# Kernel optimization log

Hardware: AMD Instinct MI355X
Metric: run time of the kernel (lower is better)

The kernel has to match this reference:

```python
import jax, jax.numpy as jnp
import numpy as np
from functools import partial

B, S, V, H, NH, NKV, M, L = 2, 2048, 51200, 1536, 24, 4, 8960, 8
DH = H // NH  # 64
EPS = 1e-6


def setup_inputs() -> dict:
    key = jax.random.key(0)
    ks = jax.random.split(key, 16)
    sc = 0.02
    w = lambda k, shape: jax.random.normal(k, shape, jnp.float32) * sc
    inp = {
        "input_ids": jax.random.randint(ks[0], (B, S), 0, V),
        "attention_mask": jnp.ones((B, S), jnp.float32),
        "embed": w(ks[1], (V, H)),
        "Wq": w(ks[2], (L, H, H)),          "bq": jnp.zeros((L, H), jnp.float32),
        "Wk": w(ks[3], (L, H, NKV * DH)),   "bk": jnp.zeros((L, NKV * DH), jnp.float32),
        "Wv": w(ks[4], (L, H, NKV * DH)),   "bv": jnp.zeros((L, NKV * DH), jnp.float32),
        "Wo": w(ks[5], (L, H, H)),
        "ln1": jnp.ones((L, H), jnp.float32),
        "ln2": jnp.ones((L, H), jnp.float32),
        "Wg": w(ks[6], (L, H, M)),
        "Wu": w(ks[7], (L, H, M)),
        "Wd": w(ks[8], (L, M, H)),
        "norm_w": jnp.ones((H,), jnp.float32),
        "W1": w(ks[9], (H, H)), "b1": jnp.zeros((H,), jnp.float32),
        "W2": w(ks[10], (H, 1)), "b2": jnp.zeros((1,), jnp.float32),
    }
    inv_freq = 1.0 / (10000.0 ** (jnp.arange(0, DH, 2, dtype=jnp.float32) / DH))
    freqs = jnp.outer(jnp.arange(S, dtype=jnp.float32), inv_freq)  # [S, DH/2]
    emb = jnp.concatenate([freqs, freqs], axis=-1)                 # [S, DH]
    inp["cos"] = jnp.cos(emb)
    inp["sin"] = jnp.sin(emb)
    return inp


def _rms(x, w):
    var = jnp.mean(x.astype(jnp.float32) ** 2, axis=-1, keepdims=True)
    return w * (x * jax.lax.rsqrt(var + EPS)).astype(x.dtype)


def _rotate_half(x):
    x1, x2 = jnp.split(x, 2, axis=-1)
    return jnp.concatenate([-x2, x1], axis=-1)


def _forward(input_ids, attention_mask, embed, Wq, bq, Wk, bk, Wv, bv, Wo,
             ln1, ln2, Wg, Wu, Wd, norm_w, W1, b1, W2, b2, cos, sin):
    scale = 1.0 / np.sqrt(DH)
    b, s = input_ids.shape
    c = cos[None, :s, None, :]  # [1,S,1,DH]
    sn = sin[None, :s, None, :]
    rope = lambda t: t * c + _rotate_half(t) * sn
    mask0 = attention_mask[:, None, None, :] == 0  # [B,1,1,S]

    def block(x, p):
        wq, bq_, wk, bk_, wv, bv_, wo, ln1w, ln2w, wg, wu, wd = p
        h = _rms(x, ln1w)
        q = (h @ wq + bq_).reshape(b, s, NH, DH)
        k = (h @ wk + bk_).reshape(b, s, NKV, DH)
        v = (h @ wv + bv_).reshape(b, s, NKV, DH)
        q, k = rope(q), rope(k)
        k = jnp.repeat(k, NH // NKV, axis=2)  # GQA expand to NH heads
        v = jnp.repeat(v, NH // NKV, axis=2)
        scores = jnp.einsum('bqhd,bkhd->bhqk', q, k) * scale
        scores = jnp.where(mask0, -1e10, scores)
        probs = jax.nn.softmax(scores, axis=-1)  # dropout: eval mode (identity)
        attn = jnp.einsum('bhqk,bkhd->bqhd', probs, v).reshape(b, s, H)
        x = x + attn @ wo
        h = _rms(x, ln2w)
        x = x + (jax.nn.sigmoid(h @ wg) * (h @ wu)) @ wd
        return x, None

    x = embed[input_ids]  # [B,S,H]
    x, _ = jax.lax.scan(block, x, (Wq, bq, Wk, bk, Wv, bv, Wo, ln1, ln2, Wg, Wu, Wd))
    x = _rms(x, norm_w)
    h = jax.nn.gelu(x @ W1 + b1, approximate=False)  # torch nn.GELU default = exact
    return h @ W2 + b2  # [B,S,1]


def reference(input_ids, attention_mask, embed, Wq, bq, Wk, bk, Wv, bv, Wo,
              ln1, ln2, Wg, Wu, Wd, norm_w, W1, b1, W2, b2, cos, sin):
    return _forward(input_ids, attention_mask, embed, Wq, bq, Wk, bk, Wv, bv, Wo,
                    ln1, ln2, Wg, Wu, Wd, norm_w, W1, b1, W2, b2, cos, sin)
```

## Files before the change

kernel.cpp:

```cpp
#include <hip/hip_runtime.h>

typedef float f32x4 __attribute__((ext_vector_type(4)));
typedef short s16x8 __attribute__((ext_vector_type(8)));
typedef unsigned short u16;
typedef unsigned short u16x4 __attribute__((ext_vector_type(4)));
typedef unsigned short u16x8 __attribute__((ext_vector_type(8)));
typedef unsigned int u32x2 __attribute__((ext_vector_type(2)));

__device__ __forceinline__ float bf2f(u16 u){ union{unsigned int i; float f;} v; v.i=((unsigned int)u)<<16; return v.f; }
__device__ __forceinline__ u16 f2bf(float f){ union{float f; unsigned int i;} v; v.f=f; return (u16)((v.i + 0x7FFFu + ((v.i>>16)&1u))>>16); }
__device__ __forceinline__ float aexp2(float x){ float r; asm("v_exp_f32 %0, %1" : "=v"(r) : "v"(x)); return r; }
__device__ __forceinline__ unsigned int cvtpk(float lo, float hi){ unsigned int r; asm("v_cvt_pk_bf16_f32 %0, %1, %2" : "=v"(r) : "v"(lo), "v"(hi)); return r; }

#define LOG2E 1.44269504089f

__device__ __forceinline__ void gld16(const void* gp, void* lp){
  __builtin_amdgcn_global_load_lds((__attribute__((address_space(1))) void*)(void*)gp,
                                   (__attribute__((address_space(3))) void*)lp, 16, 0, 0);
}

__global__ __launch_bounds__(256) void k_embed(const int* __restrict__ ids, const float* __restrict__ emb, float* __restrict__ x){
  int r = blockIdx.x;
  int id = ids[r];
  const f32x4* src = (const f32x4*)(emb + (size_t)id*1536);
  f32x4* dst = (f32x4*)(x + (size_t)r*1536);
  for (int i = threadIdx.x; i < 384; i += 256) dst[i] = src[i];
}

__global__ __launch_bounds__(256) void k_rms(const float* __restrict__ x, const float* __restrict__ w, u16* __restrict__ h){
  int r = blockIdx.x, tid = threadIdx.x;
  const f32x4* xr = (const f32x4*)(x + (size_t)r*1536);
  f32x4 v0 = xr[tid];
  float ss = v0.x*v0.x + v0.y*v0.y + v0.z*v0.z + v0.w*v0.w;
  f32x4 v1 = {0,0,0,0};
  if (tid < 128){ v1 = xr[256+tid]; ss += v1.x*v1.x + v1.y*v1.y + v1.z*v1.z + v1.w*v1.w; }
  #pragma unroll
  for (int off=32; off; off>>=1) ss += __shfl_xor(ss, off, 64);
  __shared__ float red[4];
  if ((tid&63)==0) red[tid>>6] = ss;
  __syncthreads();
  float tot = red[0]+red[1]+red[2]+red[3];
  float invr = rsqrtf(tot*(1.f/1536.f) + 1e-6f);
  const f32x4* w4 = (const f32x4*)w;
  u16x4* h4 = (u16x4*)(h + (size_t)r*1536);
  {
    f32x4 wv = w4[tid];
    u16x4 o; o.x=f2bf(v0.x*invr*wv.x); o.y=f2bf(v0.y*invr*wv.y); o.z=f2bf(v0.z*invr*wv.z); o.w=f2bf(v0.w*invr*wv.w);
    h4[tid] = o;
  }
  if (tid < 128){
    f32x4 wv = w4[256+tid];
    u16x4 o; o.x=f2bf(v1.x*invr*wv.x); o.y=f2bf(v1.y*invr*wv.y); o.z=f2bf(v1.z*invr*wv.z); o.w=f2bf(v1.w*invr*wv.w);
    h4[256+tid] = o;
  }
}

__global__ __launch_bounds__(256) void k_rms_add(float* __restrict__ x, const float* __restrict__ P, const float* __restrict__ w, u16* __restrict__ h){
  int r = blockIdx.x, tid = threadIdx.x;
  f32x4* xr = (f32x4*)(x + (size_t)r*1536);
  const f32x4* pr = (const f32x4*)(P + (size_t)r*1536);
  f32x4 v0 = xr[tid], p0 = pr[tid];
  v0.x+=p0.x; v0.y+=p0.y; v0.z+=p0.z; v0.w+=p0.w;
  xr[tid] = v0;
  float ss = v0.x*v0.x + v0.y*v0.y + v0.z*v0.z + v0.w*v0.w;
  f32x4 v1 = {0,0,0,0};
  if (tid < 128){
    v1 = xr[256+tid]; f32x4 p1 = pr[256+tid];
    v1.x+=p1.x; v1.y+=p1.y; v1.z+=p1.z; v1.w+=p1.w;
    xr[256+tid] = v1;
    ss += v1.x*v1.x + v1.y*v1.y + v1.z*v1.z + v1.w*v1.w;
  }
  #pragma unroll
  for (int off=32; off; off>>=1) ss += __shfl_xor(ss, off, 64);
  __shared__ float red[4];
  if ((tid&63)==0) red[tid>>6] = ss;
  __syncthreads();
  float tot = red[0]+red[1]+red[2]+red[3];
  float invr = rsqrtf(tot*(1.f/1536.f) + 1e-6f);
  const f32x4* w4 = (const f32x4*)w;
  u16x4* h4 = (u16x4*)(h + (size_t)r*1536);
  {
    f32x4 wv = w4[tid];
    u16x4 o; o.x=f2bf(v0.x*invr*wv.x); o.y=f2bf(v0.y*invr*wv.y); o.z=f2bf(v0.z*invr*wv.z); o.w=f2bf(v0.w*invr*wv.w);
    h4[tid] = o;
  }
  if (tid < 128){
    f32x4 wv = w4[256+tid];
    u16x4 o; o.x=f2bf(v1.x*invr*wv.x); o.y=f2bf(v1.y*invr*wv.y); o.z=f2bf(v1.z*invr*wv.z); o.w=f2bf(v1.w*invr*wv.w);
    h4[256+tid] = o;
  }
}

__device__ __forceinline__ void cvt_tile(const float* src, int K, int N, u16* dst, int k0, int n0, int roff, int mode){
  __shared__ float T[64*72];
  int tid = threadIdx.x;
  #pragma unroll
  for (int j=0;j<4;++j){
    int i = tid + j*256;
    int row = i>>4, nf = i&15;
    f32x4 vv = *(const f32x4*)(src + (size_t)(k0+row)*N + n0 + nf*4);
    *(f32x4*)&T[row*72 + nf*4] = vv;
  }
  __syncthreads();
  #pragma unroll
  for (int j=0;j<2;++j){
    int i = tid + j*256;
    int n = i>>3, kc = i&7;
    u16x8 o;
    #pragma unroll
    for (int m=0;m<8;++m) o[m] = f2bf(T[(kc*8+m)*72 + n]);
    int gn = n0 + n;
    int dr = (mode==0) ? (roff + gn) : (((gn>>4)<<5) + ((mode==2)?16:0) + (gn&15));
    *(u16x8*)(dst + (size_t)dr*K + k0 + kc*8) = o;
  }
}

__global__ __launch_bounds__(256) void k_cvt_layer(
  const float* __restrict__ Wq, const float* __restrict__ Wk, const float* __restrict__ Wv,
  const float* __restrict__ Wo, const float* __restrict__ Wg, const float* __restrict__ Wu,
  const float* __restrict__ Wd, u16* qkvt, u16* wot, u16* gut, u16* wdt)
{
  const float* src; int K, N; u16* dst; int roff=0, mode=0;
  switch (blockIdx.y){
    case 0: src=Wq; K=1536; N=1536; dst=qkvt; break;
    case 1: src=Wk; K=1536; N=256;  dst=qkvt; roff=1536; break;
    case 2: src=Wv; K=1536; N=256;  dst=qkvt; roff=1792; break;
    case 3: src=Wo; K=1536; N=1536; dst=wot;  break;
    case 4: src=Wg; K=1536; N=8960; dst=gut;  mode=1; break;
    case 5: src=Wu; K=1536; N=8960; dst=gut;  mode=2; break;
    default: src=Wd; K=8960; N=1536; dst=wdt; break;
  }
  int ntn = N>>6;
  int nt = (K>>6)*ntn;
  int t = blockIdx.x;
  if (t >= nt) return;
  cvt_tile(src, K, N, dst, (t/ntn)<<6, (t%ntn)<<6, roff, mode);
}

__global__ __launch_bounds__(256) void k_cvt_one(const float* __restrict__ src, u16* __restrict__ dst){
  int t = blockIdx.x;
  cvt_tile(src, 1536, 1536, dst, (t/24)<<6, (t%24)<<6, 0, 0);
}

#define MODE_QKV 0
#define MODE_WO 1
#define MODE_GATEUP 2
#define MODE_DOWN 3
#define MODE_W1 4

template<int MODE>
__global__ __launch_bounds__(256) void k_gemm(
  const u16* __restrict__ A, const u16* __restrict__ Bt, int K,
  int jobsPerXcd, int nc, int ksplit, int klen,
  const float* __restrict__ bq_, const float* __restrict__ bk_, const float* __restrict__ bv_,
  float* __restrict__ xio, float* __restrict__ Pf,
  const float* __restrict__ cosT, const float* __restrict__ sinT,
  u16* __restrict__ o0, u16* __restrict__ o1, u16* __restrict__ o2)
{
  int bid = blockIdx.x;
  int xcd = bid & 7, j = bid >> 3;
  int job = xcd*jobsPerXcd + (j >> 5);
  if (job >= nc*ksplit) return;
  int rowb = j & 31;
  int col = job / ksplit;
  int ks  = job - col*ksplit;
  int kbase = ks*klen;
  int nt = klen >> 5;

  __shared__ __align__(16) u16 As[4][4096], Bs[4][4096];
  int tid = threadIdx.x;
  int lane = tid & 63, w = tid >> 6;
  int wr = w >> 1, wc = w & 1;
  int row0 = rowb * 128, col0 = col * 128;
  int l15 = lane & 15, l4 = lane >> 4;
  f32x4 acc[4][4] = {};
  const u16* aBase = A + (size_t)row0*K;
  const u16* bBase = Bt + (size_t)col0*K;
  int rr0 = tid & 127, kb0 = tid >> 7;
  int kb1 = kb0 + 2;

  auto stage = [&](int bf, int kt){
    gld16(aBase + (size_t)rr0*K + kt + kb0*8, &As[bf][tid*8]);
    gld16(bBase + (size_t)rr0*K + kt + kb0*8, &Bs[bf][tid*8]);
    gld16(aBase + (size_t)rr0*K + kt + kb1*8, &As[bf][(256+tid)*8]);
    gld16(bBase + (size_t)rr0*K + kt + kb1*8, &Bs[bf][(256+tid)*8]);
  };
  stage(0, kbase); stage(1, kbase+32); stage(2, kbase+64);

  for (int t = 0; t < nt; ++t){
    if (t < nt-2)       asm volatile("s_waitcnt vmcnt(8)" ::: "memory");
    else if (t == nt-2) asm volatile("s_waitcnt vmcnt(4)" ::: "memory");
    else                asm volatile("s_waitcnt vmcnt(0)" ::: "memory");
    __builtin_amdgcn_s_barrier();
    __builtin_amdgcn_sched_barrier(0);
    if (t+3 < nt) stage((t+3)&3, kbase + (t+3)*32);
    const u16* Ab = As[t&3];
    const u16* Bb = Bs[t&3];
    s16x8 af[4], bf_[4];
    #pragma unroll
    for (int i=0;i<4;++i) af[i]  = *(const s16x8*)&Ab[((l4<<7) + wr*64 + i*16 + l15)*8];
    #pragma unroll
    for (int jj=0;jj<4;++jj) bf_[jj] = *(const s16x8*)&Bb[((l4<<7) + wc*64 + jj*16 + l15)*8];
    __builtin_amdgcn_s_setprio(1);
    #pragma unroll
    for (int i=0;i<4;++i)
      #pragma unroll
      for (int jj=0;jj<4;++jj)
        acc[i][jj] = __builtin_amdgcn_mfma_f32_16x16x32_bf16(af[i], bf_[jj], acc[i][jj], 0, 0, 0);
    __builtin_amdgcn_s_setprio(0);
  }

  #pragma unroll
  for (int i=0;i<4;++i)
    #pragma unroll
    for (int jj=0;jj<4;++jj)
      #pragma unroll
      for (int r=0;r<4;++r){
        int row = row0 + wr*64 + i*16 + l4*4 + r;
        int c   = col0 + wc*64 + jj*16 + l15;
        float v = acc[i][jj][r];
        if constexpr (MODE == MODE_QKV){
          int b = row >> 11, s = row & 2047;
          if (c < 1536){
            int d = c & 63, hd = c >> 6;
            float vv = v + bq_[c];
            float pv = acc[i][jj^2][r] + bq_[c^32];
            float cv = cosT[s*64+d], sv = sinT[s*64+d];
            float sgn = (d<32) ? -1.f : 1.f;
            float o = (vv*cv + sgn*pv*sv)*(0.125f*LOG2E);
            o0[(size_t)(b*24+hd)*131072 + (size_t)(s>>6)*4096
               + (s&63)*64 + (((d>>3)^(s&7))<<3) + (d&7)] = f2bf(o);
          } else if (c < 1792){
            int c2 = c - 1536, d = c2 & 63, kv = c2 >> 6;
            float vv = v + bk_[c2];
            float pv = acc[i][jj^2][r] + bk_[c2^32];
            float cv = cosT[s*64+d], sv = sinT[s*64+d];
            float sgn = (d<32) ? -1.f : 1.f;
            float o = vv*cv + sgn*pv*sv;
            o1[(size_t)(b*4+kv)*131072 + (size_t)(s>>6)*4096
               + (s&63)*64 + (((d>>3)^(s&7))<<3) + (d&7)] = f2bf(o);
          } else {
            int c2 = c - 1792, d = c2 & 63, kv = c2 >> 6;
            float vv = v + bv_[c2];
            o2[(size_t)(b*4+kv)*131072 + (size_t)(s>>6)*4096
               + d*64 + ((((s>>3)&7)^(d&7))<<3) + (s&7)] = f2bf(vv);
          }
        } else if constexpr (MODE == MODE_WO){
          xio[(size_t)row*1536 + c] += v;
        } else if constexpr (MODE == MODE_W1){
          v += bq_[c];
          float ge = 0.5f * v * (1.f + erff(v * 0.70710678118f));
          o0[(size_t)row*1536 + c] = f2bf(ge);
        }
      }
}

template<int MODE>
__global__ __launch_bounds__(512,2) void k_gemm256(
  const u16* __restrict__ A, const u16* __restrict__ Bt, int K,
  int nrt, int ksplit, int klen,
  float* __restrict__ xio, float* __restrict__ Pf, u16* __restrict__ o0)
{
  int bid = blockIdx.x;
  int wgid = (bid & 7)*(gridDim.x >> 3) + (bid >> 3);
  int nj = nrt*ksplit;
  int ct = wgid / nj; int r2 = wgid - ct*nj;
  int rt = r2 / ksplit; int ks = r2 - rt*ksplit;

  __shared__ __align__(16) u16 lds[2][2][16384];
  int tid = threadIdx.x;
  int lane = tid & 63, wid = tid >> 6;
  int wm = wid >> 2, wn = wid & 3;
  int l15 = lane & 15, l4 = lane >> 4;
  int row0 = rt*256, col0 = ct*256;
  int kbase = ks*klen*64;

  const u16* aB = A  + (size_t)row0*K + kbase;
  const u16* bB = Bt + (size_t)col0*K + kbase;
  int rsub = tid >> 3;
  int gsw  = (lane & 7) ^ ((lane >> 3) & 7);

  f32x4 acc[8][4] = {};

  auto stage = [&](int bf, int ktElem){
    #pragma unroll
    for (int a_=0; a_<4; ++a_){
      gld16(aB + (size_t)(a_*64 + rsub)*K + ktElem + gsw*8, &lds[bf][0][(a_*512+tid)*8]);
      gld16(bB + (size_t)(a_*64 + rsub)*K + ktElem + gsw*8, &lds[bf][1][(a_*512+tid)*8]);
    }
  };

  stage(0, 0);
  for (int t = 0; t < klen; ++t){
    asm volatile("s_waitcnt vmcnt(0)" ::: "memory");
    __builtin_amdgcn_s_barrier();
    __builtin_amdgcn_sched_barrier(0);
    if (t+1 < klen) stage((t+1)&1, (t+1)*64);
    const u16* Ab = lds[t&1][0];
    const u16* Bb = lds[t&1][1];
    #pragma unroll
    for (int ksu=0; ksu<2; ++ksu){
      s16x8 af[8], bf_[4];
      #pragma unroll
      for (int i=0;i<8;++i){
        int r = wm*128 + i*16 + l15;
        af[i] = *(const s16x8*)&Ab[r*64 + (((ksu*4 + l4) ^ (l15&7))*8)];
      }
      #pragma unroll
      for (int j=0;j<4;++j){
        int c = wn*64 + j*16 + l15;
        bf_[j] = *(const s16x8*)&Bb[c*64 + (((ksu*4 + l4) ^ (l15&7))*8)];
      }
      __builtin_amdgcn_s_setprio(1);
      #pragma unroll
      for (int i=0;i<8;++i)
        #pragma unroll
        for (int j=0;j<4;++j)
          acc[i][j] = __builtin_amdgcn_mfma_f32_16x16x32_bf16(af[i], bf_[j], acc[i][j], 0, 0, 0);
      __builtin_amdgcn_s_setprio(0);
    }
  }

  if constexpr (MODE == MODE_GATEUP){
    #pragma unroll
    for (int i=0;i<8;++i)
      #pragma unroll
      for (int j2=0;j2<4;j2+=2)
        #pragma unroll
        for (int r=0;r<4;++r){
          int row = row0 + wm*128 + i*16 + l4*4 + r;
          int cp  = col0 + wn*64 + j2*16 + l15;
          float gv = acc[i][j2][r], uv = acc[i][j2+1][r];
          float sg = 1.f/(1.f + __expf(-gv));
          int n = ((cp>>5)<<4) + (cp&15);
          o0[(size_t)row*8960 + n] = f2bf(sg*uv);
        }
  } else {
    #pragma unroll
    for (int i=0;i<8;++i)
      #pragma unroll
      for (int j=0;j<4;++j)
        #pragma unroll
        for (int r=0;r<4;++r){
          int row = row0 + wm*128 + i*16 + l4*4 + r;
          int c   = col0 + wn*64 + j*16 + l15;
          float v = acc[i][j][r];
          if (ks == 0) Pf[(size_t)row*1536 + c] = v;
          else         xio[(size_t)row*1536 + c] += v;
        }
  }
}

__global__ __launch_bounds__(256) void k_attn(
  const u16* __restrict__ q, const u16* __restrict__ k, const u16* __restrict__ v,
  const float* __restrict__ mask, u16* __restrict__ attn)
{
  __shared__ __align__(16) u16 Qs[4096];
  __shared__ __align__(16) u16 Kd[2][4096];
  __shared__ __align__(16) u16 Vd[2][4096];
  __shared__ u16 Msh[2048];
  int tid = threadIdx.x;
  int lane = tid & 63, w = tid >> 6;
  int qb = blockIdx.x;
  int bh = blockIdx.y;
  int b = bh / 24, hh = bh % 24, kv = hh / 6;
  int l15 = lane & 15, l4 = lane >> 4;
  int sw = l15 & 7;

  const u16* qhead = q + ((size_t)(b*24 + hh))*131072 + qb*4096;
  const u16* khead = k + ((size_t)(b*4  + kv))*131072;
  const u16* vhead = v + ((size_t)(b*4  + kv))*131072;

  {
    const f32x4* m4 = (const f32x4*)(mask + b*2048);
    const u16 mvis = f2bf(-4.f*LOG2E);
    const u16 mmask = f2bf(-1.4e9f);
    for (int i = tid; i < 512; i += 256){
      f32x4 mv = m4[i];
      u16x4 o;
      o.x = (mv.x==0.f) ? mmask : mvis;
      o.y = (mv.y==0.f) ? mmask : mvis;
      o.z = (mv.z==0.f) ? mmask : mvis;
      o.w = (mv.w==0.f) ? mmask : mvis;
      *(u16x4*)&Msh[i*4] = o;
    }
  }
  gld16(qhead + tid*8,       &Qs[tid*8]);
  gld16(qhead + (256+tid)*8, &Qs[(256+tid)*8]);

  auto stage = [&](int bf, int kt){
    gld16(khead + kt*4096 + tid*8,       &Kd[bf][tid*8]);
    gld16(khead + kt*4096 + (256+tid)*8, &Kd[bf][(256+tid)*8]);
    gld16(vhead + kt*4096 + tid*8,       &Vd[bf][tid*8]);
    gld16(vhead + kt*4096 + (256+tid)*8, &Vd[bf][(256+tid)*8]);
  };
  stage(0, 0);

  s16x8 aq0, aq1;
  f32x4 oacc[4] = {};
  float lsum = 0.f;
  u16* Pw = &Qs[w*1024];

  for (int t = 0; t < 32; ++t){
    asm volatile("s_waitcnt vmcnt(0)" ::: "memory");
    __builtin_amdgcn_s_barrier();
    __builtin_amdgcn_sched_barrier(0);
    if (t == 0){
      int qrow = w*16 + l15;
      aq0 = *(const s16x8*)&Qs[qrow*64 + (( l4    ^ sw)<<3)];
      aq1 = *(const s16x8*)&Qs[qrow*64 + (((4+l4) ^ sw)<<3)];
    }
    if (t+1 < 32) stage((t+1)&1, t+1);
    const u16* Kb = Kd[t&1];
    const u16* Vb = Vd[t&1];
    f32x4 sk[4] = {};
    __builtin_amdgcn_s_setprio(1);
    #pragma unroll
    for (int kn=0; kn<4; ++kn){
      int krow = kn*16 + l15;
      s16x8 a0 = *(const s16x8*)&Kb[krow*64 + (( l4    ^ sw)<<3)];
      s16x8 a1 = *(const s16x8*)&Kb[krow*64 + (((4+l4) ^ sw)<<3)];
      sk[kn] = __builtin_amdgcn_mfma_f32_16x16x32_bf16(a0, aq0, sk[kn], 0,0,0);
      sk[kn] = __builtin_amdgcn_mfma_f32_16x16x32_bf16(a1, aq1, sk[kn], 0,0,0);
    }
    __builtin_amdgcn_s_setprio(0);
    #pragma unroll
    for (int kn=0; kn<4; ++kn){
      u16x4 mv = *(const u16x4*)&Msh[t*64 + kn*16 + l4*4];
      float p0 = aexp2(sk[kn][0] + bf2f(mv.x));
      float p1 = aexp2(sk[kn][1] + bf2f(mv.y));
      float p2 = aexp2(sk[kn][2] + bf2f(mv.z));
      float p3 = aexp2(sk[kn][3] + bf2f(mv.w));
      lsum += (p0 + p1) + (p2 + p3);
      u32x2 pk; pk.x = cvtpk(p0, p1); pk.y = cvtpk(p2, p3);
      int g = kn*2 + (l4>>1);
      *(u32x2*)&Pw[l15*64 + ((g ^ sw)<<3) + (l4&1)*4] = pk;
    }
    __builtin_amdgcn_s_setprio(1);
    #pragma unroll
    for (int ksu=0; ksu<2; ++ksu){
      s16x8 ap = *(const s16x8*)&Pw[l15*64 + (((ksu*4+l4) ^ sw)<<3)];
      #pragma unroll
      for (int dg=0; dg<4; ++dg){
        s16x8 bv = *(const s16x8*)&Vb[(dg*16+l15)*64 + (((ksu*4+l4) ^ sw)<<3)];
        oacc[dg] = __builtin_amdgcn_mfma_f32_16x16x32_bf16(ap, bv, oacc[dg], 0,0,0);
      }
    }
    __builtin_amdgcn_s_setprio(0);
  }
  lsum += __shfl_xor(lsum, 16, 64);
  lsum += __shfl_xor(lsum, 32, 64);
  float invq[4];
  #pragma unroll
  for (int r=0;r<4;++r) invq[r] = 1.f / __shfl(lsum, l4*4 + r, 64);
  #pragma unroll
  for (int dg=0;dg<4;++dg)
    #pragma unroll
    for (int r=0;r<4;++r){
      int token = b*2048 + qb*64 + w*16 + l4*4 + r;
      int col = hh*64 + dg*16 + l15;
      attn[(size_t)token*1536 + col] = f2bf(oacc[dg][r] * invq[r]);
    }
}

__global__ __launch_bounds__(256) void k_gemv(const u16* __restrict__ h2, const float* __restrict__ W2, const float* __restrict__ b2, float* __restrict__ out){
  int tid = threadIdx.x, lane = tid & 63, w = tid >> 6;
  int r = blockIdx.x*4 + w;
  const u16* hr = h2 + (size_t)r*1536;
  float s = 0.f;
  #pragma unroll
  for (int i=0;i<24;++i){ int c = lane + i*64; s += bf2f(hr[c]) * W2[c]; }
  #pragma unroll
  for (int off=32; off; off>>=1) s += __shfl_xor(s, off, 64);
  if (lane == 0) out[r] = s + b2[0];
}

extern "C" void kernel_launch(void* const* d_in, const int* in_sizes, int n_in,
                              void* d_out, int out_size, void* d_ws, size_t ws_size,
                              hipStream_t stream)
{
  const int*   ids   = (const int*)d_in[0];
  const float* mask  = (const float*)d_in[1];
  const float* embed = (const float*)d_in[2];
  const float* Wq    = (const float*)d_in[3];
  const float* bq    = (const float*)d_in[4];
  const float* Wk    = (const float*)d_in[5];
  const float* bk    = (const float*)d_in[6];
  const float* Wv    = (const float*)d_in[7];
  const float* bv    = (const float*)d_in[8];
  const float* Wo    = (const float*)d_in[9];
  const float* ln1   = (const float*)d_in[10];
  const float* ln2   = (const float*)d_in[11];
  const float* Wg    = (const float*)d_in[12];
  const float* Wu    = (const float*)d_in[13];
  const float* Wd    = (const float*)d_in[14];
  const float* nw    = (const float*)d_in[15];
  const float* W1    = (const float*)d_in[16];
  const float* b1    = (const float*)d_in[17];
  const float* W2    = (const float*)d_in[18];
  const float* b2    = (const float*)d_in[19];
  const float* cosT  = (const float*)d_in[20];
  const float* sinT  = (const float*)d_in[21];

  char* ws = (char*)d_ws;
  float* x   = (float*)(ws + 0);
  u16* h     = (u16*)(ws + 25165824);
  u16* qb_   = (u16*)(ws + 37748736);
  u16* kb_   = (u16*)(ws + 50331648);
  u16* vb_   = (u16*)(ws + 52428800);
  u16* attn  = (u16*)(ws + 54525952);
  u16* g     = (u16*)(ws + 67108864);
  u16* qkvt  = (u16*)(ws + 140509184);
  u16* wot   = (u16*)(ws + 146800640);
  u16* gut   = (u16*)(ws + 151519232);
  u16* wdt   = (u16*)(ws + 206569472);
  float* Pf  = (float*)(ws + 37748736);
  (void)in_sizes; (void)n_in; (void)out_size; (void)ws_size;

  k_embed<<<4096, 256, 0, stream>>>(ids, embed, x);
  for (int l = 0; l < 8; ++l){
    k_cvt_layer<<<dim3(3360,7), 256, 0, stream>>>(
      Wq + (size_t)l*1536*1536, Wk + (size_t)l*1536*256, Wv + (size_t)l*1536*256,
      Wo + (size_t)l*1536*1536, Wg + (size_t)l*1536*8960, Wu + (size_t)l*1536*8960,
      Wd + (size_t)l*8960*1536, qkvt, wot, gut, wdt);
    if (l == 0) k_rms<<<4096, 256, 0, stream>>>(x, ln1, h);
    else        k_rms_add<<<4096, 256, 0, stream>>>(x, Pf, ln1 + l*1536, h);
    k_gemm<MODE_QKV><<<512, 256, 0, stream>>>(h, qkvt, 1536, 2, 16, 1, 1536,
        bq + l*1536, bk + l*256, bv + l*256, nullptr, nullptr, cosT, sinT, qb_, kb_, vb_);
    k_attn<<<dim3(32,48), 256, 0, stream>>>(qb_, kb_, vb_, mask, attn);
    k_gemm<MODE_WO><<<512, 256, 0, stream>>>(attn, wot, 1536, 2, 12, 1, 1536,
        nullptr, nullptr, nullptr, x, nullptr, nullptr, nullptr, nullptr, nullptr, nullptr);
    k_rms<<<4096, 256, 0, stream>>>(x, ln2 + l*1536, h);
    k_gemm256<MODE_GATEUP><<<1120, 512, 0, stream>>>(h, gut, 1536, 16, 1, 24,
        nullptr, nullptr, g);
    k_gemm256<MODE_DOWN><<<192, 512, 0, stream>>>(g, wdt, 8960, 16, 2, 70,
        x, Pf, nullptr);
  }
  k_cvt_one<<<576, 256, 0, stream>>>(W1, wot);
  k_rms_add<<<4096, 256, 0, stream>>>(x, Pf, nw, h);
  k_gemm<MODE_W1><<<512, 256, 0, stream>>>(h, wot, 1536, 2, 12, 1, 1536,
      b1, nullptr, nullptr, nullptr, nullptr, nullptr, nullptr, attn, nullptr, nullptr);
  k_gemv<<<1024, 256, 0, stream>>>(attn, W2, b2, (float*)d_out);
}
```

Baseline: 5.425 ms.

## Split GEMM tile loads into chunks interleaved with MFMA phases using partial waitcnts

The 256x256 bf16 GEMM main loop no longer waits for all global-to-LDS loads before computing. The next k-tile's B and A loads are issued in quarter chunks between four MFMA sub-phases. Partial vmcnt waits plus a mid-iteration barrier let compute on the first A rows start while the rest are still arriving. The B fragments for both k-subtiles are kept in registers and the A fragments are loaded two row-blocks at a time. This aims to hide load latency and cut peak register use, at the cost of an extra barrier per iteration and fragile hand-counted waitcnt ordering.

```diff
diff --git a/kernel.cpp b/kernel.cpp
--- a/kernel.cpp
+++ b/kernel.cpp
@@ -272,6 +272,7 @@
   int lane = tid & 63, wid = tid >> 6;
   int wm = wid >> 2, wn = wid & 3;
   int l15 = lane & 15, l4 = lane >> 4;
+  int lsw = l15 & 7;
   int row0 = rt*256, col0 = ct*256;
   int kbase = ks*klen*64;
 
@@ -282,41 +283,109 @@
 
   f32x4 acc[8][4] = {};
 
-  auto stage = [&](int bf, int ktElem){
-    #pragma unroll
-    for (int a_=0; a_<4; ++a_){
-      gld16(aB + (size_t)(a_*64 + rsub)*K + ktElem + gsw*8, &lds[bf][0][(a_*512+tid)*8]);
-      gld16(bB + (size_t)(a_*64 + rsub)*K + ktElem + gsw*8, &lds[bf][1][(a_*512+tid)*8]);
-    }
+  auto sgA = [&](int bf, int kt, int c){
+    gld16(aB + (size_t)(c*64 + rsub)*K + kt*64 + gsw*8, &lds[bf][0][(c*512+tid)*8]);
   };
-
-  stage(0, 0);
+  auto sgB = [&](int bf, int kt, int c){
+    gld16(bB + (size_t)(c*64 + rsub)*K + kt*64 + gsw*8, &lds[bf][1][(c*512+tid)*8]);
+  };
+
+  sgB(0,0,0); sgB(0,0,1); sgB(0,0,2); sgB(0,0,3);
+  sgA(0,0,0); sgA(0,0,2); sgA(0,0,1); sgA(0,0,3);
+
   for (int t = 0; t < klen; ++t){
-    asm volatile("s_waitcnt vmcnt(0)" ::: "memory");
+    int b = t & 1, nb = b ^ 1;
+    bool hasNext = (t+1 < klen);
+    const u16* Ab = lds[b][0];
+    const u16* Bb = lds[b][1];
+
+    asm volatile("s_waitcnt vmcnt(2)" ::: "memory");
     __builtin_amdgcn_s_barrier();
     __builtin_amdgcn_sched_barrier(0);
-    if (t+1 < klen) stage((t+1)&1, (t+1)*64);
-    const u16* Ab = lds[t&1][0];
-    const u16* Bb = lds[t&1][1];
-    #pragma unroll
-    for (int ksu=0; ksu<2; ++ksu){
-      s16x8 af[8], bf_[4];
-      #pragma unroll
-      for (int i=0;i<8;++i){
-        int r = wm*128 + i*16 + l15;
-        af[i] = *(const s16x8*)&Ab[r*64 + (((ksu*4 + l4) ^ (l15&7))*8)];
-      }
-      #pragma unroll
-      for (int j=0;j<4;++j){
-        int c = wn*64 + j*16 + l15;
-        bf_[j] = *(const s16x8*)&Bb[c*64 + (((ksu*4 + l4) ^ (l15&7))*8)];
-      }
+    if (hasNext){ sgB(nb, t+1, 0); sgB(nb, t+1, 1); }
+
+    s16x8 bf_[4][2];
+    #pragma unroll
+    for (int j=0;j<4;++j)
+      #pragma unroll
+      for (int ksu=0;ksu<2;++ksu)
+        bf_[j][ksu] = *(const s16x8*)&Bb[(wn*64 + j*16 + l15)*64 + (((ksu*4+l4)^lsw)<<3)];
+
+    {
+      s16x8 af[2][2];
+      #pragma unroll
+      for (int ii=0;ii<2;++ii)
+        #pragma unroll
+        for (int ksu=0;ksu<2;++ksu)
+          af[ii][ksu] = *(const s16x8*)&Ab[(wm*128 + ii*16 + l15)*64 + (((ksu*4+l4)^lsw)<<3)];
       __builtin_amdgcn_s_setprio(1);
       #pragma unroll
-      for (int i=0;i<8;++i)
+      for (int ii=0;ii<2;++ii)
         #pragma unroll
         for (int j=0;j<4;++j)
-          acc[i][j] = __builtin_amdgcn_mfma_f32_16x16x32_bf16(af[i], bf_[j], acc[i][j], 0, 0, 0);
+          #pragma unroll
+          for (int ksu=0;ksu<2;++ksu)
+            acc[ii][j] = __builtin_amdgcn_mfma_f32_16x16x32_bf16(af[ii][ksu], bf_[j][ksu], acc[ii][j], 0,0,0);
+      __builtin_amdgcn_s_setprio(0);
+    }
+    if (hasNext){ sgB(nb, t+1, 2); sgB(nb, t+1, 3); }
+    {
+      s16x8 af[2][2];
+      #pragma unroll
+      for (int ii=0;ii<2;++ii)
+        #pragma unroll
+        for (int ksu=0;ksu<2;++ksu)
+          af[ii][ksu] = *(const s16x8*)&Ab[(wm*128 + 32 + ii*16 + l15)*64 + (((ksu*4+l4)^lsw)<<3)];
+      __builtin_amdgcn_s_setprio(1);
+      #pragma unroll
+      for (int ii=0;ii<2;++ii)
+        #pragma unroll
+        for (int j=0;j<4;++j)
+          #pragma unroll
+          for (int ksu=0;ksu<2;++ksu)
+            acc[2+ii][j] = __builtin_amdgcn_mfma_f32_16x16x32_bf16(af[ii][ksu], bf_[j][ksu], acc[2+ii][j], 0,0,0);
+      __builtin_amdgcn_s_setprio(0);
+    }
+
+    if (hasNext) asm volatile("s_waitcnt vmcnt(4)" ::: "memory");
+    else         asm volatile("s_waitcnt vmcnt(0)" ::: "memory");
+    __builtin_amdgcn_s_barrier();
+    __builtin_amdgcn_sched_barrier(0);
+    if (hasNext){ sgA(nb, t+1, 0); sgA(nb, t+1, 2); }
+
+    {
+      s16x8 af[2][2];
+      #pragma unroll
+      for (int ii=0;ii<2;++ii)
+        #pragma unroll
+        for (int ksu=0;ksu<2;++ksu)
+          af[ii][ksu] = *(const s16x8*)&Ab[(wm*128 + 64 + ii*16 + l15)*64 + (((ksu*4+l4)^lsw)<<3)];
+      __builtin_amdgcn_s_setprio(1);
+      #pragma unroll
+      for (int ii=0;ii<2;++ii)
+        #pragma unroll
+        for (int j=0;j<4;++j)
+          #pragma unroll
+          for (int ksu=0;ksu<2;++ksu)
+            acc[4+ii][j] = __builtin_amdgcn_mfma_f32_16x16x32_bf16(af[ii][ksu], bf_[j][ksu], acc[4+ii][j], 0,0,0);
+      __builtin_amdgcn_s_setprio(0);
+    }
+    if (hasNext){ sgA(nb, t+1, 1); sgA(nb, t+1, 3); }
+    {
+      s16x8 af[2][2];
+      #pragma unroll
+      for (int ii=0;ii<2;++ii)
+        #pragma unroll
+        for (int ksu=0;ksu<2;++ksu)
+          af[ii][ksu] = *(const s16x8*)&Ab[(wm*128 + 96 + ii*16 + l15)*64 + (((ksu*4+l4)^lsw)<<3)];
+      __builtin_amdgcn_s_setprio(1);
+      #pragma unroll
+      for (int ii=0;ii<2;++ii)
+        #pragma unroll
+        for (int j=0;j<4;++j)
+          #pragma unroll
+          for (int ksu=0;ksu<2;++ksu)
+            acc[6+ii][j] = __builtin_amdgcn_mfma_f32_16x16x32_bf16(af[ii][ksu], bf_[j][ksu], acc[6+ii][j], 0,0,0);
       __builtin_amdgcn_s_setprio(0);
     }
   }
```

After: 5.425 ms. Within noise of the previous version (+0.0%).
